# Performance work log

Hardware: AMD Instinct MI355X
Metric: run time of the kernel (lower is better)

## Reference

```python
import jax, jax.numpy as jnp
import numpy as np

B, S, H = 16, 2048, 768
D_VOCAB, C_VOCAB, U_VOCAB = 512, 512, 50000
D_DIM, C_DIM, MIX_CD = 128, 128, 128


def setup_inputs() -> dict:
    key = jax.random.key(0)
    ks = jax.random.split(key, 11)
    initrange = 0.1
    return {
        "seqs": jax.random.normal(ks[0], (B, S, H), dtype=jnp.float32),
        "d": jax.random.randint(ks[1], (B, S - 1), 0, D_VOCAB),
        "c": jax.random.randint(ks[2], (B, S - 1), 0, C_VOCAB),
        "u": jax.random.randint(ks[3], (B, S), 0, U_VOCAB),
        # embedding tables (torch init: uniform(-0.1, 0.1))
        "E_d": jax.random.uniform(ks[4], (D_VOCAB, D_DIM), jnp.float32, -initrange, initrange),
        "E_c": jax.random.uniform(ks[5], (C_VOCAB, C_DIM), jnp.float32, -initrange, initrange),
        "E_u": jax.random.uniform(ks[6], (U_VOCAB, H), jnp.float32, -initrange, initrange),
        # Linear weights, torch layout [out, in], no bias
        "W_cd": jax.random.normal(ks[7], (MIX_CD, D_DIM + C_DIM), dtype=jnp.float32) * 0.02,
        "W_hid": jax.random.normal(ks[8], (H, 2 * H), dtype=jnp.float32) * 0.02,
        "W_cdh": jax.random.normal(ks[9], (H, MIX_CD + H), dtype=jnp.float32) * 0.02,
    }


def reference(seqs, d, c, u, E_d, E_c, E_u, W_cd, W_hid, W_cdh):
    de = E_d[d]                      # [B, S-1, d_dim]
    ce = E_c[c]                      # [B, S-1, c_dim]
    ue = E_u[u]                      # [B, S, H]
    seqs_u = seqs + ue               # [B, S, H]
    # relu(Linear(cat(d, c)))
    d_c = jax.nn.relu(jnp.einsum('bsi,oi->bso', jnp.concatenate([de, ce], axis=-1), W_cd))
    # adjacent pairs: stack([seqs_u[:, i:i+2]]) then flatten last two dims == cat of shifted views
    pairs = jnp.concatenate([seqs_u[:, :-1], seqs_u[:, 1:]], axis=-1)  # [B, S-1, 2H]
    ph = jax.nn.relu(jnp.einsum('bsi,oi->bso', pairs, W_hid))          # [B, S-1, H]
    m = jax.nn.relu(jnp.einsum('bsi,oi->bso', jnp.concatenate([ph, d_c], axis=-1), W_cdh))  # [B, S-1, H]
    # loop: seqs_u[:, i] += (m[:, i] if i < S-1) + (m[:, i-1] if i > 1)
    # -> two shifted vectorized adds (note: i > 1, so m[:, 0] is NOT added at i=1)
    out = seqs_u.at[:, :-1].add(m)
    out = out.at[:, 2:].add(m[:, 1:])
    return out
```

## Files before the change

### kernel.cpp

```cpp
#include <hip/hip_runtime.h>
#include <hip/hip_bf16.h>
#include <cstdint>
#include <cstddef>

#define B_SZ   16
#define S_LEN  2048
#define H_DIM  768
#define M_ROWS (B_SZ * (S_LEN - 1))

typedef __attribute__((ext_vector_type(8))) __bf16 bf16x8;
typedef __attribute__((ext_vector_type(8))) unsigned short ushort8;
typedef __attribute__((ext_vector_type(4))) float floatx4;

__device__ __forceinline__ float bf2f(unsigned short h) {
  union { unsigned u; float f; } v; v.u = ((unsigned)h) << 16; return v.f;
}
__device__ __forceinline__ unsigned short f2bf(float f) {
  union { float f; unsigned u; } v; v.f = f;
  unsigned u = v.u + 0x7fffu + ((v.u >> 16) & 1u);
  return (unsigned short)(u >> 16);
}

__device__ __forceinline__ void load_lds16(const void* g, void* l) {
  __builtin_amdgcn_global_load_lds(
      (const __attribute__((address_space(1))) void*)g,
      (__attribute__((address_space(3))) void*)l, 16, 0, 0);
}

#define N_ED   (512 * 128)
#define N_EC   (512 * 128)
#define N_WCD  (128 * 256)
#define N_WHID (768 * 1536)
#define N_WCDH (768 * 896)
#define N_CONV (N_ED + N_EC + N_WCD + N_WHID + N_WCDH)

__global__ void convert_weights_kernel(const float* __restrict__ Ed,
                                       const float* __restrict__ Ec,
                                       const float* __restrict__ Wcd,
                                       const float* __restrict__ Whid,
                                       const float* __restrict__ Wcdh,
                                       unsigned short* __restrict__ ed_b,
                                       unsigned short* __restrict__ ec_b,
                                       unsigned short* __restrict__ wcd_b,
                                       unsigned short* __restrict__ whid_b,
                                       unsigned short* __restrict__ wcdh_b) {
  long i = ((long)blockIdx.x * blockDim.x + threadIdx.x) * 8;
  const float* s; unsigned short* dst; long off;
  if (i < N_ED)                            { s = Ed;   dst = ed_b;   off = i; }
  else if (i < N_ED + N_EC)                { s = Ec;   dst = ec_b;   off = i - N_ED; }
  else if (i < N_ED + N_EC + N_WCD)        { s = Wcd;  dst = wcd_b;  off = i - (N_ED + N_EC); }
  else if (i < N_ED + N_EC + N_WCD + N_WHID) { s = Whid; dst = whid_b; off = i - (N_ED + N_EC + N_WCD); }
  else                                     { s = Wcdh; dst = wcdh_b; off = i - (N_ED + N_EC + N_WCD + N_WHID); }
  floatx4 v0 = *(const floatx4*)(s + off);
  floatx4 v1 = *(const floatx4*)(s + off + 4);
  ushort8 o;
#pragma unroll
  for (int t = 0; t < 4; ++t) { o[t] = f2bf(v0[t]); o[t + 4] = f2bf(v1[t]); }
  *(ushort8*)(dst + off) = o;
}

__global__ void embed_add_kernel(const float* __restrict__ seqs,
                                 const int* __restrict__ u,
                                 const float* __restrict__ Eu,
                                 float* __restrict__ out,
                                 unsigned short* __restrict__ sub, int nchunks) {
  int c = blockIdx.x * blockDim.x + threadIdx.x;
  if (c >= nchunks) return;
  int row = c / 96;
  int hc  = c - row * 96;
  int uid = u[row];
  const floatx4* sp = (const floatx4*)seqs + (size_t)c * 2;
  const floatx4* ep = (const floatx4*)(Eu + (size_t)uid * H_DIM + hc * 8);
  floatx4 a0 = sp[0], a1 = sp[1];
  floatx4 b0 = ep[0], b1 = ep[1];
  floatx4 r0, r1; ushort8 ob;
#pragma unroll
  for (int t = 0; t < 4; ++t) {
    r0[t] = a0[t] + b0[t];
    r1[t] = a1[t] + b1[t];
    ob[t] = f2bf(r0[t]); ob[t + 4] = f2bf(r1[t]);
  }
  floatx4* op = (floatx4*)out + (size_t)c * 2;
  op[0] = r0; op[1] = r1;
  *((ushort8*)sub + c) = ob;
}

template <int MODE, int K, int LDW, int NOUT>
__global__ __launch_bounds__(256)
void gemm_nt_relu(const unsigned short* __restrict__ A0,
                  const unsigned short* __restrict__ A1,
                  const int* __restrict__ idx0,
                  const int* __restrict__ idx1,
                  const unsigned short* __restrict__ W,
                  unsigned short* __restrict__ out) {
  constexpr int NT = NOUT / 128;
  const int bm = blockIdx.x / NT;
  const int bn = blockIdx.x - bm * NT;

  __shared__ unsigned short As[128 * 64];
  __shared__ unsigned short Ws[128 * 64];

  const int tid  = threadIdx.x;
  const int lane = tid & 63;
  const int wave = tid >> 6;
  const int lrow = lane >> 3;
  const int cc   = lane & 7;
  const int wm   = wave >> 1, wn = wave & 1;
  const int m16  = lane & 15, quad = lane >> 4;

  floatx4 acc[4][4] = {};

  for (int kt = 0; kt < K / 64; ++kt) {
    const int colbase = kt * 64;
#pragma unroll
    for (int it = 0; it < 4; ++it) {
      int row = it * 32 + wave * 8 + lrow;
      int n = bm * 128 + row;
      if (n >= M_ROWS) n = M_ROWS - 1;
      const unsigned short* g;
      if constexpr (MODE == 0) {
        if (colbase < 128) g = A0 + (size_t)idx0[n] * 128 + colbase + cc * 8;
        else               g = A1 + (size_t)idx1[n] * 128 + (colbase - 128) + cc * 8;
      } else if constexpr (MODE == 1) {
        int b = n / (S_LEN - 1);
        int s = n - b * (S_LEN - 1);
        int grow = b * S_LEN + s + (colbase >= H_DIM ? 1 : 0);
        int gcol = (colbase >= H_DIM ? colbase - H_DIM : colbase) + cc * 8;
        g = A0 + (size_t)grow * H_DIM + gcol;
      } else {
        if (colbase < H_DIM) g = A0 + (size_t)n * H_DIM + colbase + cc * 8;
        else                 g = A1 + (size_t)n * 128 + (colbase - H_DIM) + cc * 8;
      }
      load_lds16(g, &As[(it * 256 + wave * 64) * 8]);

      int wrow = bn * 128 + row;
      const unsigned short* gw = W + (size_t)wrow * LDW + colbase + cc * 8;
      load_lds16(gw, &Ws[(it * 256 + wave * 64) * 8]);
    }
    __syncthreads();

#pragma unroll
    for (int kk = 0; kk < 64; kk += 32) {
      bf16x8 a[4], b[4];
#pragma unroll
      for (int i = 0; i < 4; ++i)
        a[i] = *(const bf16x8*)&As[(wm * 64 + i * 16 + m16) * 64 + kk + quad * 8];
#pragma unroll
      for (int j = 0; j < 4; ++j)
        b[j] = *(const bf16x8*)&Ws[(wn * 64 + j * 16 + m16) * 64 + kk + quad * 8];
#pragma unroll
      for (int i = 0; i < 4; ++i)
#pragma unroll
        for (int j = 0; j < 4; ++j)
          acc[i][j] = __builtin_amdgcn_mfma_f32_16x16x32_bf16(a[i], b[j], acc[i][j], 0, 0, 0);
    }
    __syncthreads();
  }

#pragma unroll
  for (int i = 0; i < 4; ++i) {
#pragma unroll
    for (int r = 0; r < 4; ++r) {
      int row = bm * 128 + wm * 64 + i * 16 + quad * 4 + r;
      if (row < M_ROWS) {
#pragma unroll
        for (int j = 0; j < 4; ++j) {
          int col = bn * 128 + wn * 64 + j * 16 + m16;
          out[(size_t)row * NOUT + col] = f2bf(fmaxf(acc[i][j][r], 0.0f));
        }
      }
    }
  }
}

__global__ void final_add_kernel(const unsigned short* __restrict__ mm,
                                 float* __restrict__ out, int nchunks) {
  int c = blockIdx.x * blockDim.x + threadIdx.x;
  if (c >= nchunks) return;
  int row = c / 96;
  int hc  = c - row * 96;
  int b = row >> 11;
  int s = row & (S_LEN - 1);
  floatx4* op = (floatx4*)out + (size_t)c * 2;
  floatx4 v0 = op[0], v1 = op[1];
  int mrow = b * (S_LEN - 1) + s;
  if (s < S_LEN - 1) {
    ushort8 x = *(const ushort8*)(mm + (size_t)mrow * H_DIM + hc * 8);
#pragma unroll
    for (int t = 0; t < 4; ++t) { v0[t] += bf2f(x[t]); v1[t] += bf2f(x[t + 4]); }
  }
  if (s >= 2) {
    ushort8 x = *(const ushort8*)(mm + (size_t)(mrow - 1) * H_DIM + hc * 8);
#pragma unroll
    for (int t = 0; t < 4; ++t) { v0[t] += bf2f(x[t]); v1[t] += bf2f(x[t + 4]); }
  }
  op[0] = v0; op[1] = v1;
}

extern "C" void kernel_launch(void* const* d_in, const int* in_sizes, int n_in,
                              void* d_out, int out_size, void* d_ws, size_t ws_size,
                              hipStream_t stream) {
  const float* seqs  = (const float*)d_in[0];
  const int*   d_idx = (const int*)d_in[1];
  const int*   c_idx = (const int*)d_in[2];
  const int*   u_idx = (const int*)d_in[3];
  const float* E_d   = (const float*)d_in[4];
  const float* E_c   = (const float*)d_in[5];
  const float* E_u   = (const float*)d_in[6];
  const float* W_cd  = (const float*)d_in[7];
  const float* W_hid = (const float*)d_in[8];
  const float* W_cdh = (const float*)d_in[9];
  float* out = (float*)d_out;

  unsigned short* sub   = (unsigned short*)d_ws;
  unsigned short* ph    = sub   + (size_t)B_SZ * S_LEN * H_DIM;
  unsigned short* mmb   = ph    + (size_t)M_ROWS * H_DIM;
  unsigned short* dc    = mmb   + (size_t)M_ROWS * H_DIM;
  unsigned short* ed_b  = dc    + (size_t)M_ROWS * 128;
  unsigned short* ec_b  = ed_b  + N_ED;
  unsigned short* wcd_b = ec_b  + N_EC;
  unsigned short* whid_b = wcd_b + N_WCD;
  unsigned short* wcdh_b = whid_b + N_WHID;

  const int nchunks = B_SZ * S_LEN * (H_DIM / 8);
  const int mtiles = (M_ROWS + 127) / 128;

  convert_weights_kernel<<<N_CONV / (256 * 8), 256, 0, stream>>>(
      E_d, E_c, W_cd, W_hid, W_cdh, ed_b, ec_b, wcd_b, whid_b, wcdh_b);
  embed_add_kernel<<<(nchunks + 255) / 256, 256, 0, stream>>>(seqs, u_idx, E_u, out, sub, nchunks);
  gemm_nt_relu<0, 256, 256, 128><<<mtiles * 1, 256, 0, stream>>>(ed_b, ec_b, d_idx, c_idx, wcd_b, dc);
  gemm_nt_relu<1, 1536, 1536, 768><<<mtiles * 6, 256, 0, stream>>>(sub, nullptr, nullptr, nullptr, whid_b, ph);
  gemm_nt_relu<2, 896, 896, 768><<<mtiles * 6, 256, 0, stream>>>(ph, dc, nullptr, nullptr, wcdh_b, mmb);
  final_add_kernel<<<(nchunks + 255) / 256, 256, 0, stream>>>(mmb, out, nchunks);
}
```

Before: 576.5 us.

## Swizzle LDS tiles with XOR and remap workgroups across XCDs in GEMM

Global-to-LDS loads now write each 16-byte chunk to a column position XORed with the row index, and the MFMA operand reads apply the matching XOR. This is meant to remove LDS bank conflicts on the strided row reads. Workgroup IDs are also remapped so consecutive tiles land on the same XCD, which should improve L2 reuse of shared A and W tiles. The swizzle assumes 8-row groups line up with the XOR pattern, and the remap assumes the hardware assigns workgroups to XCDs round-robin.

```diff
diff --git a/kernel.cpp b/kernel.cpp
--- a/kernel.cpp
+++ b/kernel.cpp
@@ -94,8 +94,13 @@
                   const unsigned short* __restrict__ W,
                   unsigned short* __restrict__ out) {
   constexpr int NT = NOUT / 128;
-  const int bm = blockIdx.x / NT;
-  const int bn = blockIdx.x - bm * NT;
+
+  const int nwg = gridDim.x;
+  const int q = nwg >> 3, r = nwg & 7;
+  const int xcd = blockIdx.x & 7, lid = blockIdx.x >> 3;
+  const int wgid = (xcd < r ? xcd * (q + 1) : r * (q + 1) + (xcd - r) * q) + lid;
+  const int bm = wgid / NT;
+  const int bn = wgid - bm * NT;
 
   __shared__ unsigned short As[128 * 64];
   __shared__ unsigned short Ws[128 * 64];
@@ -105,8 +110,10 @@
   const int wave = tid >> 6;
   const int lrow = lane >> 3;
   const int cc   = lane & 7;
+  const int scc  = cc ^ lrow;
   const int wm   = wave >> 1, wn = wave & 1;
   const int m16  = lane & 15, quad = lane >> 4;
+  const int rxor = m16 & 7;
 
   floatx4 acc[4][4] = {};
 
@@ -119,35 +126,40 @@
       if (n >= M_ROWS) n = M_ROWS - 1;
       const unsigned short* g;
       if constexpr (MODE == 0) {
-        if (colbase < 128) g = A0 + (size_t)idx0[n] * 128 + colbase + cc * 8;
-        else               g = A1 + (size_t)idx1[n] * 128 + (colbase - 128) + cc * 8;
+        if (colbase < 128) g = A0 + (size_t)idx0[n] * 128 + colbase + scc * 8;
+        else               g = A1 + (size_t)idx1[n] * 128 + (colbase - 128) + scc * 8;
       } else if constexpr (MODE == 1) {
         int b = n / (S_LEN - 1);
         int s = n - b * (S_LEN - 1);
         int grow = b * S_LEN + s + (colbase >= H_DIM ? 1 : 0);
-        int gcol = (colbase >= H_DIM ? colbase - H_DIM : colbase) + cc * 8;
+        int gcol = (colbase >= H_DIM ? colbase - H_DIM : colbase) + scc * 8;
         g = A0 + (size_t)grow * H_DIM + gcol;
       } else {
-        if (colbase < H_DIM) g = A0 + (size_t)n * H_DIM + colbase + cc * 8;
-        else                 g = A1 + (size_t)n * 128 + (colbase - H_DIM) + cc * 8;
+        if (colbase < H_DIM) g = A0 + (size_t)n * H_DIM + colbase + scc * 8;
+        else                 g = A1 + (size_t)n * 128 + (colbase - H_DIM) + scc * 8;
       }
       load_lds16(g, &As[(it * 256 + wave * 64) * 8]);
 
       int wrow = bn * 128 + row;
-      const unsigned short* gw = W + (size_t)wrow * LDW + colbase + cc * 8;
+      const unsigned short* gw = W + (size_t)wrow * LDW + colbase + scc * 8;
       load_lds16(gw, &Ws[(it * 256 + wave * 64) * 8]);
     }
     __syncthreads();
 
 #pragma unroll
     for (int kk = 0; kk < 64; kk += 32) {
+      const int k8 = kk >> 3;
       bf16x8 a[4], b[4];
 #pragma unroll
-      for (int i = 0; i < 4; ++i)
-        a[i] = *(const bf16x8*)&As[(wm * 64 + i * 16 + m16) * 64 + kk + quad * 8];
-#pragma unroll
-      for (int j = 0; j < 4; ++j)
-        b[j] = *(const bf16x8*)&Ws[(wn * 64 + j * 16 + m16) * 64 + kk + quad * 8];
+      for (int i = 0; i < 4; ++i) {
+        int rr = wm * 64 + i * 16 + m16;
+        a[i] = *(const bf16x8*)&As[rr * 64 + (((k8 + quad) ^ rxor) << 3)];
+      }
+#pragma unroll
+      for (int j = 0; j < 4; ++j) {
+        int rr = wn * 64 + j * 16 + m16;
+        b[j] = *(const bf16x8*)&Ws[rr * 64 + (((k8 + quad) ^ rxor) << 3)];
+      }
 #pragma unroll
       for (int i = 0; i < 4; ++i)
 #pragma unroll
@@ -160,13 +172,13 @@
 #pragma unroll
   for (int i = 0; i < 4; ++i) {
 #pragma unroll
-    for (int r = 0; r < 4; ++r) {
-      int row = bm * 128 + wm * 64 + i * 16 + quad * 4 + r;
+    for (int r2 = 0; r2 < 4; ++r2) {
+      int row = bm * 128 + wm * 64 + i * 16 + quad * 4 + r2;
       if (row < M_ROWS) {
 #pragma unroll
         for (int j = 0; j < 4; ++j) {
           int col = bn * 128 + wn * 64 + j * 16 + m16;
-          out[(size_t)row * NOUT + col] = f2bf(fmaxf(acc[i][j][r], 0.0f));
+          out[(size_t)row * NOUT + col] = f2bf(fmaxf(acc[i][j][r2], 0.0f));
         }
       }
     }
```

Result: faster. 552.5 us (-4.2%).
